# Kernel tuning notes

Hardware: AMD Instinct MI355X
Metric: run time of the kernel (lower is better)

The kernel has to match this reference:

```python
import jax, jax.numpy as jnp
import numpy as np

B, T, D, N = 2, 2048, 2048, 16
H = D // N          # 128 head dim
F = H // 2          # 64 rotary frequencies


def setup_inputs() -> dict:
    key = jax.random.key(0)
    k1, k2, k3 = jax.random.split(key, 3)
    x = jax.random.normal(k1, (B, T, D), dtype=jnp.float32)
    # causal mask [T, T], True = attend
    mask = jnp.tril(jnp.ones((T, T), dtype=bool))
    # RoPE tables: freqs = 1 / 10000^(2i/H), angles = t * freqs
    freqs = 1.0 / (10000.0 ** (jnp.arange(0, H, 2, dtype=jnp.float32) / H))  # [F]
    angles = jnp.arange(T, dtype=jnp.float32)[:, None] * freqs[None, :]      # [T, F]
    cos, sin = jnp.cos(angles), jnp.sin(angles)
    w_attn = jax.random.normal(k2, (D, 3 * D), dtype=jnp.float32) * 0.02
    w_out = jax.random.normal(k3, (D, D), dtype=jnp.float32) * 0.02
    return {"x": x, "mask": mask, "cos": cos, "sin": sin,
            "w_attn": w_attn, "w_out": w_out}


def _rope(x_BNTH, cos_TF, sin_TF):
    # complex multiply on adjacent pairs of the head dim
    x = x_BNTH.reshape(*x_BNTH.shape[:-1], F, 2)  # [B,N,T,F,2]
    xr, xi = x[..., 0], x[..., 1]
    out_r = xr * cos_TF - xi * sin_TF             # broadcast [T,F] over [B,N,T,F]
    out_i = xr * sin_TF + xi * cos_TF
    return jnp.stack([out_r, out_i], axis=-1).reshape(x_BNTH.shape)


def reference(x, mask, cos, sin, w_attn, w_out):
    qkv = x @ w_attn                                  # [B,T,3D]
    q, k, v = jnp.split(qkv, 3, axis=-1)
    def to_heads(z):
        return z.reshape(B, T, N, H).transpose(0, 2, 1, 3)  # [B,N,T,H]
    q, k, v = to_heads(q), to_heads(k), to_heads(v)
    # NOTE: this module applies rotary embedding to k AND v (not q), per source
    k = _rope(k, cos, sin)
    v = _rope(v, cos, sin)
    scale = 1.0 / jnp.sqrt(jnp.asarray(H, dtype=q.dtype))
    scores = jnp.einsum('bnqh,bnkh->bnqk', q, k) * scale  # [B,N,T,T]
    scores = jnp.where(mask, scores, jnp.finfo(scores.dtype).min)
    attn = jax.nn.softmax(scores, axis=-1)
    o = jnp.einsum('bnqk,bnkh->bnqh', attn, v)            # [B,N,T,H]
    o = o.transpose(0, 2, 1, 3).reshape(B, T, D)          # [B,T,D]
    return o @ w_out
```

## Files before the change

kernel.cpp:

```cpp
#include <hip/hip_runtime.h>

typedef unsigned short u16;
typedef unsigned int u32;

#define B_ 2
#define T_ 2048
#define D_ 2048
#define N_ 16
#define H_ 128
#define F_ 64
#define QSCALE 0.12751743226f

typedef __attribute__((ext_vector_type(8))) __bf16 bf16x8;
typedef __attribute__((ext_vector_type(8))) short s16x8;
typedef __attribute__((ext_vector_type(4))) float f32x4;
typedef __attribute__((ext_vector_type(4))) u16 u16x4;
typedef __attribute__((ext_vector_type(4))) u32 u32x4;

__device__ inline u16 f2bf(float f) {
    union { float f; u32 u; } v; v.f = f;
    u32 u = v.u;
    u32 r = (u + 0x7FFFu + ((u >> 16) & 1u)) >> 16;
    return (u16)r;
}
__device__ inline float bf2f(u16 h) {
    union { u32 u; float f; } v; v.u = ((u32)h) << 16;
    return v.f;
}
__device__ inline bf16x8 ld8(const u16* p) {
    s16x8 r = *reinterpret_cast<const s16x8*>(p);
    return __builtin_bit_cast(bf16x8, r);
}
__device__ inline f32x4 mfma16(bf16x8 a, bf16x8 b, f32x4 c) {
    return __builtin_amdgcn_mfma_f32_16x16x32_bf16(a, b, c, 0, 0, 0);
}
__device__ inline void gload_lds16(const u16* g, u16* l) {
    __builtin_amdgcn_global_load_lds(
        (const __attribute__((address_space(1))) void*)g,
        (__attribute__((address_space(3))) void*)l, 16, 0, 0);
}
__device__ inline float exp2fast(float x) {
    float r;
    asm("v_exp_f32 %0, %1" : "=v"(r) : "v"(x));
    return r;
}
__device__ inline u32 cvtpk(float lo, float hi) {
    u32 r;
    asm("v_cvt_pk_bf16_f32 %0, %1, %2" : "=v"(r) : "v"(lo), "v"(hi));
    return r;
}

__global__ __launch_bounds__(256) void prep(const float* __restrict__ x,
                                            u16* __restrict__ xb,
                                            const float* __restrict__ wA,
                                            u16* __restrict__ wAt,
                                            const float* __restrict__ wO,
                                            u16* __restrict__ wOt) {
    __shared__ float tile[64][65];
    const int bid = blockIdx.x;
    const int tid = threadIdx.x;

    if (bid < 4096) {
        int i = (bid * 256 + tid) * 8;
        float4 a = *reinterpret_cast<const float4*>(x + i);
        float4 b = *reinterpret_cast<const float4*>(x + i + 4);
        s16x8 o;
        o[0] = (short)f2bf(a.x); o[1] = (short)f2bf(a.y);
        o[2] = (short)f2bf(a.z); o[3] = (short)f2bf(a.w);
        o[4] = (short)f2bf(b.x); o[5] = (short)f2bf(b.y);
        o[6] = (short)f2bf(b.z); o[7] = (short)f2bf(b.w);
        *reinterpret_cast<s16x8*>(xb + i) = o;
        return;
    }

    const float* in;
    u16* out;
    int Nc, bx, by;
    if (bid < 4096 + 3072) {
        int idx = bid - 4096;
        in = wA; out = wAt; Nc = 3 * D_;
        bx = idx % 96; by = idx / 96;
    } else {
        int idx = bid - 7168;
        in = wO; out = wOt; Nc = D_;
        bx = idx & 31; by = idx >> 5;
    }
    const int K = D_;
    int n0 = bx * 64, k0 = by * 64;
    int rr = tid >> 4;
    int cc = (tid & 15) * 4;
#pragma unroll
    for (int it = 0; it < 4; ++it) {
        int kk = it * 16 + rr;
        float4 v = *reinterpret_cast<const float4*>(in + (size_t)(k0 + kk) * Nc + n0 + cc);
        tile[kk][cc] = v.x; tile[kk][cc + 1] = v.y; tile[kk][cc + 2] = v.z; tile[kk][cc + 3] = v.w;
    }
    __syncthreads();
#pragma unroll
    for (int it = 0; it < 4; ++it) {
        int nn = it * 16 + rr;
        u16x4 o;
#pragma unroll
        for (int j = 0; j < 4; ++j) o[j] = f2bf(tile[cc + j][nn]);
        *reinterpret_cast<u16x4*>(out + (size_t)(n0 + nn) * K + k0 + cc) = o;
    }
}

#define BM 128
#define BN 128
#define BKg 32

__global__ __launch_bounds__(256) void gemm_bt(const u16* __restrict__ A,
                                               const u16* __restrict__ Bt,
                                               u16* __restrict__ Cb,
                                               float* __restrict__ Cf,
                                               int M, int Nn, int K, int out_f32) {
    __shared__ __align__(16) u16 As[2][BM * BKg];
    __shared__ __align__(16) u16 Bs[2][BM * BKg];
    const int tid = threadIdx.x;
    const int wave = tid >> 6, lane = tid & 63;

    const int NW = (Nn >> 7) >> 3;
    const int bid = blockIdx.x;
    const int xcd = bid & 7, idx = bid >> 3;
    const int nloc = idx % NW, mloc = idx / NW;
    const int m0 = mloc * BM, n0 = (xcd * NW + nloc) * BN;

    const int lrow = lane >> 2, lcol = (lane & 3) * 8;
    const int wr = (wave >> 1) * 64, wc = (wave & 1) * 64;
    const int g = lane >> 4, c0 = lane & 15;

    f32x4 acc[4][4] = {};

    const int NT = K / BKg;

    auto stage = [&](int buf, int kt) {
        const int k0 = kt * BKg;
#pragma unroll
        for (int j = 0; j < 2; ++j) {
            const int c = wave + j * 4;
            gload_lds16(A + (size_t)(m0 + c * 16 + lrow) * K + k0 + lcol, &As[buf][c * 512]);
            gload_lds16(Bt + (size_t)(n0 + c * 16 + lrow) * K + k0 + lcol, &Bs[buf][c * 512]);
        }
    };

    stage(0, 0);
    __syncthreads();

    for (int t = 0; t < NT; ++t) {
        const int cur = t & 1;
        if (t + 1 < NT) stage(cur ^ 1, t + 1);
        bf16x8 af[4], bfr[4];
#pragma unroll
        for (int i = 0; i < 4; ++i) {
            af[i]  = ld8(&As[cur][(wr + i * 16 + c0) * BKg + g * 8]);
            bfr[i] = ld8(&Bs[cur][(wc + i * 16 + c0) * BKg + g * 8]);
        }
#pragma unroll
        for (int i = 0; i < 4; ++i)
#pragma unroll
            for (int j = 0; j < 4; ++j)
                acc[i][j] = mfma16(af[i], bfr[j], acc[i][j]);
        __syncthreads();
    }

#pragma unroll
    for (int i = 0; i < 4; ++i)
#pragma unroll
        for (int j = 0; j < 4; ++j)
#pragma unroll
            for (int r = 0; r < 4; ++r) {
                int row = m0 + wr + i * 16 + g * 4 + r;
                int col = n0 + wc + j * 16 + c0;
                float v = acc[i][j][r];
                if (out_f32) Cf[(size_t)row * Nn + col] = v;
                else         Cb[(size_t)row * Nn + col] = f2bf(v);
            }
}

__global__ __launch_bounds__(256) void rope_split(const u16* __restrict__ qkv,
                                                  const float* __restrict__ cosT,
                                                  const float* __restrict__ sinT,
                                                  u16* __restrict__ qs,
                                                  u16* __restrict__ kr,
                                                  u16* __restrict__ vt) {
    __shared__ u16 vtile[64][129];
    int bi = blockIdx.x;
    int hn = bi >> 5;
    int tt = bi & 31;
    int b = hn >> 4, n = hn & 15;
    int t0 = tt * 64;
    int tid = threadIdx.x;
    int tl = tid >> 2;
    int h0 = (tid & 3) * 32;
    int t = t0 + tl;
    const u16* row = qkv + ((size_t)(b * T_ + t)) * (3 * D_);

#pragma unroll
    for (int u = 0; u < 4; ++u) {
        s16x8 raw = *reinterpret_cast<const s16x8*>(row + n * H_ + h0 + u * 8);
        s16x8 o;
#pragma unroll
        for (int e = 0; e < 8; ++e) o[e] = (short)f2bf(bf2f((u16)raw[e]) * QSCALE);
        *reinterpret_cast<s16x8*>(qs + ((size_t)hn * T_ + t) * H_ + h0 + u * 8) = o;
    }

    float cbuf[16], sbuf[16];
    const float* cr = cosT + (size_t)t * F_ + h0 / 2;
    const float* sr = sinT + (size_t)t * F_ + h0 / 2;
#pragma unroll
    for (int u = 0; u < 4; ++u) {
        float4 c4 = *reinterpret_cast<const float4*>(cr + u * 4);
        float4 s4 = *reinterpret_cast<const float4*>(sr + u * 4);
        cbuf[u * 4 + 0] = c4.x; cbuf[u * 4 + 1] = c4.y; cbuf[u * 4 + 2] = c4.z; cbuf[u * 4 + 3] = c4.w;
        sbuf[u * 4 + 0] = s4.x; sbuf[u * 4 + 1] = s4.y; sbuf[u * 4 + 2] = s4.z; sbuf[u * 4 + 3] = s4.w;
    }

#pragma unroll
    for (int u = 0; u < 4; ++u) {
        s16x8 raw = *reinterpret_cast<const s16x8*>(row + D_ + n * H_ + h0 + u * 8);
        s16x8 o;
#pragma unroll
        for (int p = 0; p < 4; ++p) {
            float xr = bf2f((u16)raw[2 * p]), xi = bf2f((u16)raw[2 * p + 1]);
            float cc = cbuf[u * 4 + p], ss = sbuf[u * 4 + p];
            o[2 * p]     = (short)f2bf(xr * cc - xi * ss);
            o[2 * p + 1] = (short)f2bf(xr * ss + xi * cc);
        }
        *reinterpret_cast<s16x8*>(kr + ((size_t)hn * T_ + t) * H_ + h0 + u * 8) = o;
    }

#pragma unroll
    for (int u = 0; u < 4; ++u) {
        s16x8 raw = *reinterpret_cast<const s16x8*>(row + 2 * D_ + n * H_ + h0 + u * 8);
#pragma unroll
        for (int p = 0; p < 4; ++p) {
            float xr = bf2f((u16)raw[2 * p]), xi = bf2f((u16)raw[2 * p + 1]);
            float cc = cbuf[u * 4 + p], ss = sbuf[u * 4 + p];
            vtile[tl][h0 + u * 8 + 2 * p]     = f2bf(xr * cc - xi * ss);
            vtile[tl][h0 + u * 8 + 2 * p + 1] = f2bf(xr * ss + xi * cc);
        }
    }
    __syncthreads();

    int hrow = tid >> 1;
    int th = (tid & 1) * 32;
    u16 tmp[32];
#pragma unroll
    for (int i = 0; i < 32; ++i) tmp[i] = vtile[th + i][hrow];
    u16* dst = vt + ((size_t)(hn * H_ + hrow)) * T_ + t0 + th;
#pragma unroll
    for (int u = 0; u < 4; ++u) {
        s16x8 o;
#pragma unroll
        for (int e = 0; e < 8; ++e) o[e] = (short)tmp[u * 8 + e];
        *reinterpret_cast<s16x8*>(dst + u * 8) = o;
    }
}

__global__ __launch_bounds__(256, 2) void attn_fwd(const u16* __restrict__ qs,
                                                   const u16* __restrict__ kr,
                                                   const u16* __restrict__ vt,
                                                   u16* __restrict__ ob) {
    __shared__ __align__(16) u16 Ks[2][8192];
    __shared__ __align__(16) u16 Vs[2][8192];

    const int wave = threadIdx.x >> 6, lane = threadIdx.x & 63;
    const int g = lane >> 4, c0 = lane & 15;

    const int wg = blockIdx.x;
    const int orig = (wg & 7) * 64 + (wg >> 3);
    const int hn = orig >> 4;
    const int qt = orig & 15;
    const int hA = 31 - qt;
    const int hB = qt;

    const u16* qh = qs + (size_t)hn * T_ * H_;
    const u16* kh = kr + (size_t)hn * T_ * H_;
    const u16* vh = vt + (size_t)hn * H_ * T_;

    const int q0[2] = { hA * 64 + wave * 16, hB * 64 + wave * 16 };

    bf16x8 qf[2][4];
#pragma unroll
    for (int i = 0; i < 2; ++i)
#pragma unroll
        for (int kf = 0; kf < 4; ++kf)
            qf[i][kf] = ld8(qh + (size_t)(q0[i] + c0) * H_ + kf * 32 + g * 8);

    f32x4 o[2][8] = {};
    float m[2] = { -1e30f, -1e30f };
    float l[2] = { 0.0f, 0.0f };

    const int nt = hA + 1;

    auto stage = [&](int buf, int t) {
        const int kv0 = t * 64;
#pragma unroll
        for (int j = 0; j < 4; ++j) {
            int ra = wave * 16 + j * 4 + (lane >> 4);
            int ca = ((lane & 15) * 8) ^ ((ra & 7) << 3);
            gload_lds16(kh + (size_t)(kv0 + ra) * H_ + ca, &Ks[buf][wave * 2048 + j * 512]);
            int rv = wave * 32 + j * 8 + (lane >> 3);
            int cv = ((lane & 7) * 8) ^ ((rv & 7) << 3);
            gload_lds16(vh + (size_t)rv * T_ + kv0 + cv, &Vs[buf][wave * 2048 + j * 512]);
        }
    };

    stage(0, 0);
    __syncthreads();

    const int srcA = ((g & 1) * 2) * 16 + c0;
    const int srcB = srcA + 16;
    const int sel  = g >> 1;

    for (int t = 0; t < nt; ++t) {
        const int cur = t & 1;
        const int kv0 = t * 64;
        if (t + 1 < nt) stage(cur ^ 1, t + 1);

        const bool a0 = kv0 < q0[0] + 16;
        const bool a1 = kv0 < q0[1] + 16;

        f32x4 s[2][4] = {};
        __builtin_amdgcn_s_setprio(1);
#pragma unroll
        for (int cc = 0; cc < 4; ++cc) {
            const int krow = cc * 16 + c0;
#pragma unroll
            for (int kf = 0; kf < 4; ++kf) {
                bf16x8 kfr = ld8(&Ks[cur][krow * 128 + ((kf * 32 + g * 8) ^ ((krow & 7) << 3))]);
                if (a0) s[0][cc] = mfma16(kfr, qf[0][kf], s[0][cc]);
                if (a1) s[1][cc] = mfma16(kfr, qf[1][kf], s[1][cc]);
            }
        }
        __builtin_amdgcn_s_setprio(0);

        bf16x8 pb[2][2];
#pragma unroll
        for (int i = 0; i < 2; ++i) {
            const bool act = i ? a1 : a0;
            if (!act) continue;
            const int qrow = q0[i] + c0;
            if (kv0 + 63 > q0[i]) {
#pragma unroll
                for (int cc = 0; cc < 4; ++cc) {
                    int kloc = kv0 + cc * 16 + g * 4;
#pragma unroll
                    for (int r = 0; r < 4; ++r)
                        if (kloc + r > qrow) s[i][cc][r] = -1e30f;
                }
            }
            float pmax = s[i][0][0];
#pragma unroll
            for (int cc = 0; cc < 4; ++cc)
#pragma unroll
                for (int r = 0; r < 4; ++r) pmax = fmaxf(pmax, s[i][cc][r]);
            if (!__all(pmax <= m[i] + 8.0f)) {
                pmax = fmaxf(pmax, __shfl_xor(pmax, 16));
                pmax = fmaxf(pmax, __shfl_xor(pmax, 32));
                float mn = fmaxf(m[i], pmax);
                float al = exp2fast(m[i] - mn);
                m[i] = mn;
                l[i] *= al;
#pragma unroll
                for (int hf = 0; hf < 8; ++hf)
#pragma unroll
                    for (int r = 0; r < 4; ++r) o[i][hf][r] *= al;
            }
            u32 w[4][2];
#pragma unroll
            for (int cc = 0; cc < 4; ++cc) {
                float p0 = exp2fast(s[i][cc][0] - m[i]);
                float p1 = exp2fast(s[i][cc][1] - m[i]);
                float p2 = exp2fast(s[i][cc][2] - m[i]);
                float p3 = exp2fast(s[i][cc][3] - m[i]);
                l[i] += (p0 + p1) + (p2 + p3);
                w[cc][0] = cvtpk(p0, p1);
                w[cc][1] = cvtpk(p2, p3);
            }
#pragma unroll
            for (int ks2 = 0; ks2 < 2; ++ks2) {
                u32 r00 = __shfl(w[ks2 * 2 + 0][0], srcA);
                u32 r01 = __shfl(w[ks2 * 2 + 0][1], srcA);
                u32 r02 = __shfl(w[ks2 * 2 + 0][0], srcB);
                u32 r03 = __shfl(w[ks2 * 2 + 0][1], srcB);
                u32 r10 = __shfl(w[ks2 * 2 + 1][0], srcA);
                u32 r11 = __shfl(w[ks2 * 2 + 1][1], srcA);
                u32 r12 = __shfl(w[ks2 * 2 + 1][0], srcB);
                u32 r13 = __shfl(w[ks2 * 2 + 1][1], srcB);
                u32x4 wv;
                wv[0] = sel ? r10 : r00;
                wv[1] = sel ? r11 : r01;
                wv[2] = sel ? r12 : r02;
                wv[3] = sel ? r13 : r03;
                pb[i][ks2] = __builtin_bit_cast(bf16x8, wv);
            }
        }

        __builtin_amdgcn_s_setprio(1);
#pragma unroll
        for (int hf = 0; hf < 8; ++hf) {
            const int vrow = hf * 16 + c0;
#pragma unroll
            for (int ks2 = 0; ks2 < 2; ++ks2) {
                bf16x8 vfr = ld8(&Vs[cur][vrow * 64 + ((ks2 * 32 + g * 8) ^ ((vrow & 7) << 3))]);
                if (a0) o[0][hf] = mfma16(vfr, pb[0][ks2], o[0][hf]);
                if (a1) o[1][hf] = mfma16(vfr, pb[1][ks2], o[1][hf]);
            }
        }
        __builtin_amdgcn_s_setprio(0);
        __syncthreads();
    }

    const int bb = hn >> 4, nn = hn & 15;
#pragma unroll
    for (int i = 0; i < 2; ++i) {
        float lt = l[i] + __shfl_xor(l[i], 16);
        lt += __shfl_xor(lt, 32);
        float inv = 1.0f / lt;
        const size_t rowoff = ((size_t)(bb * T_ + q0[i] + c0)) * D_ + nn * H_ + g * 4;
#pragma unroll
        for (int hf = 0; hf < 8; ++hf) {
            u16x4 pk;
#pragma unroll
            for (int r = 0; r < 4; ++r) pk[r] = f2bf(o[i][hf][r] * inv);
            *reinterpret_cast<u16x4*>(ob + rowoff + hf * 16) = pk;
        }
    }
}

extern "C" void kernel_launch(void* const* d_in, const int* in_sizes, int n_in,
                              void* d_out, int out_size, void* d_ws, size_t ws_size,
                              hipStream_t stream) {
    const float* x      = (const float*)d_in[0];
    const float* cosT   = (const float*)d_in[2];
    const float* sinT   = (const float*)d_in[3];
    const float* w_attn = (const float*)d_in[4];
    const float* w_out  = (const float*)d_in[5];
    float* out = (float*)d_out;

    char* ws = (char*)d_ws;
    u16* xb  = (u16*)(ws + 0);
    u16* wat = (u16*)(ws + 16777216);
    u16* wot = (u16*)(ws + 41943040);
    u16* qkv = (u16*)(ws + 50331648);
    u16* qsb = (u16*)(ws + 100663296);
    u16* krb = (u16*)(ws + 117440512);
    u16* vtb = (u16*)(ws + 134217728);
    u16* obf = (u16*)(ws + 0);

    prep<<<8192, 256, 0, stream>>>(x, xb, w_attn, wat, w_out, wot);
    gemm_bt<<<dim3((3 * D_ / BN) * (B_ * T_ / BM)), 256, 0, stream>>>(xb, wat, qkv, nullptr,
                                                                      B_ * T_, 3 * D_, D_, 0);
    rope_split<<<B_ * N_ * (T_ / 64), 256, 0, stream>>>(qkv, cosT, sinT, qsb, krb, vtb);
    attn_fwd<<<B_ * N_ * (T_ / 128), 256, 0, stream>>>(qsb, krb, vtb, obf);
    gemm_bt<<<dim3((D_ / BN) * (B_ * T_ / BM)), 256, 0, stream>>>(obf, wot, nullptr, out,
                                                                  B_ * T_, D_, D_, 1);
}
```

Baseline: 309.8 us.

## Split attention into one query tile per block with 32-key tiles

Drops the paired-tile (hA/hB) causal load-balancing scheme. Each workgroup now handles a single 64-row query tile, and twice as many blocks are launched, heaviest tiles first. The K/V tiles shrink to 32 keys, which halves LDS, and launch bounds go up to 4 blocks per CU to raise occupancy. The costs are lost Q reuse across two tiles per block, more K/V reloads across blocks, more loop iterations with barriers, and less MFMA work per sync.

Result: slower. 328.7 us (+6.1%).

```diff
diff --git a/kernel.cpp b/kernel.cpp
--- a/kernel.cpp
+++ b/kernel.cpp
@@ -258,52 +258,48 @@
     }
 }
 
-__global__ __launch_bounds__(256, 2) void attn_fwd(const u16* __restrict__ qs,
+__global__ __launch_bounds__(256, 4) void attn_fwd(const u16* __restrict__ qs,
                                                    const u16* __restrict__ kr,
                                                    const u16* __restrict__ vt,
                                                    u16* __restrict__ ob) {
-    __shared__ __align__(16) u16 Ks[2][8192];
-    __shared__ __align__(16) u16 Vs[2][8192];
+    __shared__ __align__(16) u16 Ks[2][4096];
+    __shared__ __align__(16) u16 Vs[2][4096];
 
     const int wave = threadIdx.x >> 6, lane = threadIdx.x & 63;
     const int g = lane >> 4, c0 = lane & 15;
 
     const int wg = blockIdx.x;
-    const int orig = (wg & 7) * 64 + (wg >> 3);
-    const int hn = orig >> 4;
-    const int qt = orig & 15;
-    const int hA = 31 - qt;
-    const int hB = qt;
+    const int orig = (wg & 7) * 128 + (wg >> 3);
+    const int hn = orig >> 5;
+    const int h = 31 - (orig & 31);
 
     const u16* qh = qs + (size_t)hn * T_ * H_;
     const u16* kh = kr + (size_t)hn * T_ * H_;
     const u16* vh = vt + (size_t)hn * H_ * T_;
 
-    const int q0[2] = { hA * 64 + wave * 16, hB * 64 + wave * 16 };
-
-    bf16x8 qf[2][4];
-#pragma unroll
-    for (int i = 0; i < 2; ++i)
-#pragma unroll
-        for (int kf = 0; kf < 4; ++kf)
-            qf[i][kf] = ld8(qh + (size_t)(q0[i] + c0) * H_ + kf * 32 + g * 8);
-
-    f32x4 o[2][8] = {};
-    float m[2] = { -1e30f, -1e30f };
-    float l[2] = { 0.0f, 0.0f };
-
-    const int nt = hA + 1;
+    const int q0 = h * 64 + wave * 16;
+
+    bf16x8 qf[4];
+#pragma unroll
+    for (int kf = 0; kf < 4; ++kf)
+        qf[kf] = ld8(qh + (size_t)(q0 + c0) * H_ + kf * 32 + g * 8);
+
+    f32x4 o[8] = {};
+    float m = -1e30f;
+    float l = 0.0f;
+
+    const int nt = 2 * h + 2;
 
     auto stage = [&](int buf, int t) {
-        const int kv0 = t * 64;
-#pragma unroll
-        for (int j = 0; j < 4; ++j) {
-            int ra = wave * 16 + j * 4 + (lane >> 4);
+        const int kv0 = t * 32;
+#pragma unroll
+        for (int j = 0; j < 2; ++j) {
+            int ra = wave * 8 + j * 4 + (lane >> 4);
             int ca = ((lane & 15) * 8) ^ ((ra & 7) << 3);
-            gload_lds16(kh + (size_t)(kv0 + ra) * H_ + ca, &Ks[buf][wave * 2048 + j * 512]);
-            int rv = wave * 32 + j * 8 + (lane >> 3);
-            int cv = ((lane & 7) * 8) ^ ((rv & 7) << 3);
-            gload_lds16(vh + (size_t)rv * T_ + kv0 + cv, &Vs[buf][wave * 2048 + j * 512]);
+            gload_lds16(kh + (size_t)(kv0 + ra) * H_ + ca, &Ks[buf][wave * 1024 + j * 512]);
+            int rv = wave * 32 + j * 16 + (lane >> 2);
+            int cv = ((lane & 3) * 8) ^ ((rv & 3) << 3);
+            gload_lds16(vh + (size_t)rv * T_ + kv0 + cv, &Vs[buf][wave * 1024 + j * 512]);
         }
     };
 
@@ -316,117 +312,102 @@
 
     for (int t = 0; t < nt; ++t) {
         const int cur = t & 1;
-        const int kv0 = t * 64;
+        const int kv0 = t * 32;
         if (t + 1 < nt) stage(cur ^ 1, t + 1);
 
-        const bool a0 = kv0 < q0[0] + 16;
-        const bool a1 = kv0 < q0[1] + 16;
-
-        f32x4 s[2][4] = {};
+        const bool act = kv0 < q0 + 16;
+
+        f32x4 s[2] = {};
         __builtin_amdgcn_s_setprio(1);
 #pragma unroll
-        for (int cc = 0; cc < 4; ++cc) {
+        for (int cc = 0; cc < 2; ++cc) {
             const int krow = cc * 16 + c0;
 #pragma unroll
             for (int kf = 0; kf < 4; ++kf) {
                 bf16x8 kfr = ld8(&Ks[cur][krow * 128 + ((kf * 32 + g * 8) ^ ((krow & 7) << 3))]);
-                if (a0) s[0][cc] = mfma16(kfr, qf[0][kf], s[0][cc]);
-                if (a1) s[1][cc] = mfma16(kfr, qf[1][kf], s[1][cc]);
+                if (act) s[cc] = mfma16(kfr, qf[kf], s[cc]);
             }
         }
         __builtin_amdgcn_s_setprio(0);
 
-        bf16x8 pb[2][2];
-#pragma unroll
-        for (int i = 0; i < 2; ++i) {
-            const bool act = i ? a1 : a0;
-            if (!act) continue;
-            const int qrow = q0[i] + c0;
-            if (kv0 + 63 > q0[i]) {
-#pragma unroll
-                for (int cc = 0; cc < 4; ++cc) {
+        bf16x8 pb;
+        if (act) {
+            const int qrow = q0 + c0;
+            if (kv0 + 31 > q0) {
+#pragma unroll
+                for (int cc = 0; cc < 2; ++cc) {
                     int kloc = kv0 + cc * 16 + g * 4;
 #pragma unroll
                     for (int r = 0; r < 4; ++r)
-                        if (kloc + r > qrow) s[i][cc][r] = -1e30f;
+                        if (kloc + r > qrow) s[cc][r] = -1e30f;
                 }
             }
-            float pmax = s[i][0][0];
-#pragma unroll
-            for (int cc = 0; cc < 4; ++cc)
-#pragma unroll
-                for (int r = 0; r < 4; ++r) pmax = fmaxf(pmax, s[i][cc][r]);
-            if (!__all(pmax <= m[i] + 8.0f)) {
+            float pmax = s[0][0];
+#pragma unroll
+            for (int cc = 0; cc < 2; ++cc)
+#pragma unroll
+                for (int r = 0; r < 4; ++r) pmax = fmaxf(pmax, s[cc][r]);
+            if (!__all(pmax <= m + 8.0f)) {
                 pmax = fmaxf(pmax, __shfl_xor(pmax, 16));
                 pmax = fmaxf(pmax, __shfl_xor(pmax, 32));
-                float mn = fmaxf(m[i], pmax);
-                float al = exp2fast(m[i] - mn);
-                m[i] = mn;
-                l[i] *= al;
+                float mn = fmaxf(m, pmax);
+                float al = exp2fast(m - mn);
+                m = mn;
+                l *= al;
 #pragma unroll
                 for (int hf = 0; hf < 8; ++hf)
 #pragma unroll
-                    for (int r = 0; r < 4; ++r) o[i][hf][r] *= al;
+                    for (int r = 0; r < 4; ++r) o[hf][r] *= al;
             }
-            u32 w[4][2];
-#pragma unroll
-            for (int cc = 0; cc < 4; ++cc) {
-                float p0 = exp2fast(s[i][cc][0] - m[i]);
-                float p1 = exp2fast(s[i][cc][1] - m[i]);
-                float p2 = exp2fast(s[i][cc][2] - m[i]);
-                float p3 = exp2fast(s[i][cc][3] - m[i]);
-                l[i] += (p0 + p1) + (p2 + p3);
+            u32 w[2][2];
+#pragma unroll
+            for (int cc = 0; cc < 2; ++cc) {
+                float p0 = exp2fast(s[cc][0] - m);
+                float p1 = exp2fast(s[cc][1] - m);
+                float p2 = exp2fast(s[cc][2] - m);
+                float p3 = exp2fast(s[cc][3] - m);
+                l += (p0 + p1) + (p2 + p3);
                 w[cc][0] = cvtpk(p0, p1);
                 w[cc][1] = cvtpk(p2, p3);
             }
-#pragma unroll
-            for (int ks2 = 0; ks2 < 2; ++ks2) {
-                u32 r00 = __shfl(w[ks2 * 2 + 0][0], srcA);
-                u32 r01 = __shfl(w[ks2 * 2 + 0][1], srcA);
-                u32 r02 = __shfl(w[ks2 * 2 + 0][0], srcB);
-                u32 r03 = __shfl(w[ks2 * 2 + 0][1], srcB);
-                u32 r10 = __shfl(w[ks2 * 2 + 1][0], srcA);
-                u32 r11 = __shfl(w[ks2 * 2 + 1][1], srcA);
-                u32 r12 = __shfl(w[ks2 * 2 + 1][0], srcB);
-                u32 r13 = __shfl(w[ks2 * 2 + 1][1], srcB);
-                u32x4 wv;
-                wv[0] = sel ? r10 : r00;
-                wv[1] = sel ? r11 : r01;
-                wv[2] = sel ? r12 : r02;
-                wv[3] = sel ? r13 : r03;
-                pb[i][ks2] = __builtin_bit_cast(bf16x8, wv);
-            }
+            u32 r00 = __shfl(w[0][0], srcA);
+            u32 r01 = __shfl(w[0][1], srcA);
+            u32 r02 = __shfl(w[0][0], srcB);
+            u32 r03 = __shfl(w[0][1], srcB);
+            u32 r10 = __shfl(w[1][0], srcA);
+            u32 r11 = __shfl(w[1][1], srcA);
+            u32 r12 = __shfl(w[1][0], srcB);
+            u32 r13 = __shfl(w[1][1], srcB);
+            u32x4 wv;
+            wv[0] = sel ? r10 : r00;
+            wv[1] = sel ? r11 : r01;
+            wv[2] = sel ? r12 : r02;
+            wv[3] = sel ? r13 : r03;
+            pb = __builtin_bit_cast(bf16x8, wv);
         }
 
         __builtin_amdgcn_s_setprio(1);
 #pragma unroll
         for (int hf = 0; hf < 8; ++hf) {
             const int vrow = hf * 16 + c0;
-#pragma unroll
-            for (int ks2 = 0; ks2 < 2; ++ks2) {
-                bf16x8 vfr = ld8(&Vs[cur][vrow * 64 + ((ks2 * 32 + g * 8) ^ ((vrow & 7) << 3))]);
-                if (a0) o[0][hf] = mfma16(vfr, pb[0][ks2], o[0][hf]);
-                if (a1) o[1][hf] = mfma16(vfr, pb[1][ks2], o[1][hf]);
-            }
+            bf16x8 vfr = ld8(&Vs[cur][vrow * 32 + ((g * 8) ^ ((vrow & 3) << 3))]);
+            if (act) o[hf] = mfma16(vfr, pb, o[hf]);
         }
         __builtin_amdgcn_s_setprio(0);
         __syncthreads();
     }
 
     const int bb = hn >> 4, nn = hn & 15;
-#pragma unroll
-    for (int i = 0; i < 2; ++i) {
-        float lt = l[i] + __shfl_xor(l[i], 16);
-        lt += __shfl_xor(lt, 32);
-        float inv = 1.0f / lt;
-        const size_t rowoff = ((size_t)(bb * T_ + q0[i] + c0)) * D_ + nn * H_ + g * 4;
-#pragma unroll
-        for (int hf = 0; hf < 8; ++hf) {
-            u16x4 pk;
-#pragma unroll
-            for (int r = 0; r < 4; ++r) pk[r] = f2bf(o[i][hf][r] * inv);
-            *reinterpret_cast<u16x4*>(ob + rowoff + hf * 16) = pk;
-        }
+    float lt = l + __shfl_xor(l, 16);
+    lt += __shfl_xor(lt, 32);
+    float inv = 1.0f / lt;
+    const size_t rowoff = ((size_t)(bb * T_ + q0 + c0)) * D_ + nn * H_ + g * 4;
+#pragma unroll
+    for (int hf = 0; hf < 8; ++hf) {
+        u16x4 pk;
+#pragma unroll
+        for (int r = 0; r < 4; ++r) pk[r] = f2bf(o[hf][r] * inv);
+        *reinterpret_cast<u16x4*>(ob + rowoff + hf * 16) = pk;
     }
 }
 
@@ -454,7 +435,7 @@
     gemm_bt<<<dim3((3 * D_ / BN) * (B_ * T_ / BM)), 256, 0, stream>>>(xb, wat, qkv, nullptr,
                                                                       B_ * T_, 3 * D_, D_, 0);
     rope_split<<<B_ * N_ * (T_ / 64), 256, 0, stream>>>(qkv, cosT, sinT, qsb, krb, vtb);
-    attn_fwd<<<B_ * N_ * (T_ / 128), 256, 0, stream>>>(qsb, krb, vtb, obf);
+    attn_fwd<<<B_ * N_ * (T_ / 64), 256, 0, stream>>>(qsb, krb, vtb, obf);
     gemm_bt<<<dim3((D_ / BN) * (B_ * T_ / BM)), 256, 0, stream>>>(obf, wot, nullptr, out,
                                                                   B_ * T_, D_, D_, 1);
 }
```
